# Kernel tuning notes

Measured on AMD Instinct MI355X. Metric: run time of the kernel, lower is better.

## Reference

```python
import jax, jax.numpy as jnp
import numpy as np

N_NODES = 40000            # num nodes (maybe_num_nodes)
E = 2_560_000              # input edges
SENTINEL = N_NODES * N_NODES  # key for masked-out edges; sorts last; fits int32 (1.6e9 < 2^31)


def setup_inputs() -> dict:
    key = jax.random.key(0)
    k1, k2 = jax.random.split(key)
    edge_index = jax.random.randint(k1, (2, E), 0, N_NODES, dtype=jnp.int32)
    edge_attr = jax.random.uniform(k2, (E,), dtype=jnp.float32)
    t = jnp.full((1,), 0.5, dtype=jnp.float32)  # learnable threshold parameter
    return {"edge_index": edge_index, "edge_attr": edge_attr, "t": t}


def reference(edge_index, edge_attr, t):
    """Threshold mask -> symmetrize -> coalesce (sort by (row,col), sum duplicates).

    JAX has static shapes, so compaction is expressed as masking: dropped edges get
    key=SENTINEL (sorts last) and attr contribution 0. Returns padded outputs of
    fixed size 2E plus the count of valid (unique, kept) edges. Invalid slots have
    edge_index == -1 and edge_attr == 0.
    """
    row, col = edge_index[0], edge_index[1]
    mask = edge_attr <= t[0]                      # [E] bool
    # symmetrize: stack (row,col) and (col,row), duplicate attrs  -> [2E]
    r2 = jnp.concatenate([row, col])
    c2 = jnp.concatenate([col, row])
    a2 = jnp.concatenate([edge_attr, edge_attr])
    m2 = jnp.concatenate([mask, mask])
    # coalesce: linearize key = row*N + col, sort, segment-sum duplicates
    key = jnp.where(m2, r2 * N_NODES + c2, SENTINEL)   # [2E] int32
    order = jnp.argsort(key)
    key_s = key[order]
    a_s = jnp.where(m2, a2, 0.0)[order]
    E2 = key_s.shape[0]
    new_seg = jnp.concatenate([jnp.ones((1,), bool), key_s[1:] != key_s[:-1]])
    seg = jnp.cumsum(new_seg.astype(jnp.int32)) - 1    # segment id per sorted edge
    vals = jax.ops.segment_sum(a_s, seg, num_segments=E2, indices_are_sorted=True)
    uk = jnp.full((E2,), SENTINEL, dtype=key_s.dtype).at[seg].set(key_s)
    valid = uk < SENTINEL
    out_row = jnp.where(valid, uk // N_NODES, -1)
    out_col = jnp.where(valid, uk % N_NODES, -1)
    edge_index_out = jnp.stack([out_row, out_col])     # [2, 2E] padded with -1
    edge_attr_out = jnp.where(valid, vals, 0.0)        # [2E]   padded with 0
    num_edges = jnp.sum(valid.astype(jnp.int32))
    return edge_index_out, edge_attr_out, num_edges
```

## Files before the change

kernel.cpp:

```cpp
#include <hip/hip_runtime.h>
#include <stdint.h>

#define NN 40000
#define E_IN 2560000
#define E2 5120000
#define NFINE 2500
#define NSB 20
#define SB_SHIFT 11
#define FINES_PER_SB 128
#define P2_TILES 17
#define P2_TILE 8192
#define SBCAP 135168
#define CAPB 1280
#define CSTR 16
#define P1_BLOCKS 625
#define P1_THREADS 1024
#define OF_BLOCKS 1250

typedef unsigned long long ull;

__global__ void k_init(int* __restrict__ sbCursor, int* __restrict__ fineCursor) {
    int tid = threadIdx.x;
    for (int f = tid; f < NFINE; f += 256) fineCursor[f * CSTR] = f * CAPB;
    if (tid < NSB) sbCursor[tid * CSTR] = tid * SBCAP;
}

__global__ void __launch_bounds__(P1_THREADS) k_part1(const int* __restrict__ ei,
                                                      const float* __restrict__ ea,
                                                      const float* __restrict__ t,
                                                      int* __restrict__ sbCursor,
                                                      ull* __restrict__ pairs1) {
    __shared__ ull staged[8192];
    __shared__ int cntO[NSB * 8];
    __shared__ int off[NSB + 1], wb[NSB * 8], gbase[NSB];
    int tid = threadIdx.x;
    int oct = (tid >> 3) & 7;
    if (tid < NSB * 8) cntO[tid] = 0;
    __syncthreads();
    float t0 = t[0];
    int i0 = blockIdx.x * 4096 + tid * 4;

    float4 a4 = *(const float4*)(ea + i0);
    int4 r4 = *(const int4*)(ei + i0);
    int4 c4 = *(const int4*)(ei + E_IN + i0);
    float av[4] = {a4.x, a4.y, a4.z, a4.w};
    int rv[4] = {r4.x, r4.y, r4.z, r4.w};
    int cv[4] = {c4.x, c4.y, c4.z, c4.w};

    ull eA[4], eB[4];
    int rkA[4], rkB[4];
    bool keep[4];
#pragma unroll
    for (int k = 0; k < 4; k++) {
        keep[k] = (av[k] <= t0);
        if (keep[k]) {
            unsigned ab = __float_as_uint(av[k]);
            eA[k] = ((ull)(unsigned)rv[k] << 48) | ((ull)(unsigned)cv[k] << 32) | ab;
            eB[k] = ((ull)(unsigned)cv[k] << 48) | ((ull)(unsigned)rv[k] << 32) | ab;
            rkA[k] = atomicAdd(&cntO[((rv[k] >> SB_SHIFT) << 3) | oct], 1);
            rkB[k] = atomicAdd(&cntO[((cv[k] >> SB_SHIFT) << 3) | oct], 1);
        }
    }
    __syncthreads();
    if (tid < NSB) {
        int s = tid;
        int c[8], tot = 0;
#pragma unroll
        for (int o = 0; o < 8; o++) { c[o] = cntO[s * 8 + o]; tot += c[o]; }
        int incl = tot;
#pragma unroll
        for (int d = 1; d < 32; d <<= 1) {
            int y = __shfl_up(incl, d, 64);
            if (s >= d) incl += y;
        }
        int o0 = incl - tot;
        off[s] = o0;
        if (s == NSB - 1) off[NSB] = incl;
        int acc = o0;
#pragma unroll
        for (int o = 0; o < 8; o++) { wb[s * 8 + o] = acc; acc += c[o]; }
        gbase[s] = atomicAdd(&sbCursor[s * CSTR], tot);
    }
    __syncthreads();
#pragma unroll
    for (int k = 0; k < 4; k++) {
        if (keep[k]) {
            staged[wb[(((int)(eA[k] >> 59)) << 3) | oct] + rkA[k]] = eA[k];
            staged[wb[(((int)(eB[k] >> 59)) << 3) | oct] + rkB[k]] = eB[k];
        }
    }
    __syncthreads();
    int total = off[NSB];
    for (int i = tid; i < total; i += P1_THREADS) {
        ull e = staged[i];
        int sb = (int)(e >> 59);
        pairs1[gbase[sb] + (i - off[sb])] = e;
    }
}

__global__ void __launch_bounds__(1024) k_part2(const int* __restrict__ sbCursor,
                                                int* __restrict__ fineCursor,
                                                const ull* __restrict__ pairs1,
                                                ull* __restrict__ pairs2) {
    int sb = blockIdx.x / P2_TILES;
    int tile = blockIdx.x % P2_TILES;
    int regionBase = sb * SBCAP;
    int len = sbCursor[sb * CSTR] - regionBase;
    if (len > SBCAP) len = SBCAP;
    int start = tile * P2_TILE;
    if (start >= len) return;
    int cntT = len - start; if (cntT > P2_TILE) cntT = P2_TILE;
    const ull* src = pairs1 + regionBase + start;

    int fineFirst = sb * FINES_PER_SB;
    int nF = NFINE - fineFirst; if (nF > FINES_PER_SB) nF = FINES_PER_SB;

    __shared__ ull staged[P2_TILE];
    __shared__ int cnt[FINES_PER_SB], off[FINES_PER_SB + 1], gbase[FINES_PER_SB], wsum2[2];
    int tid = threadIdx.x;
    if (tid < FINES_PER_SB) { cnt[tid] = 0; gbase[tid] = 0; }
    __syncthreads();

    ull e[8];
    int rk[8];
#pragma unroll
    for (int k = 0; k < 8; k++) {
        int i = tid + k * 1024;
        if (i < cntT) {
            e[k] = src[i];
            rk[k] = atomicAdd(&cnt[(int)(e[k] >> 52) & 127], 1);
        }
    }
    __syncthreads();
    int x = 0, incl = 0;
    if (tid < FINES_PER_SB) {
        x = cnt[tid];
        incl = x;
        int lane = tid & 63;
#pragma unroll
        for (int d = 1; d < 64; d <<= 1) {
            int y = __shfl_up(incl, d, 64);
            if (lane >= d) incl += y;
        }
        if (lane == 63) wsum2[tid >> 6] = incl;
    }
    __syncthreads();
    if (tid == 0) { int a = wsum2[0]; wsum2[0] = 0; wsum2[1] = a; }
    __syncthreads();
    if (tid < FINES_PER_SB) {
        off[tid] = wsum2[tid >> 6] + incl - x;
        if (tid == FINES_PER_SB - 1) off[FINES_PER_SB] = wsum2[1] + incl;
        if (tid < nF) gbase[tid] = atomicAdd(&fineCursor[(fineFirst + tid) * CSTR], x);
    }
    __syncthreads();
#pragma unroll
    for (int k = 0; k < 8; k++) {
        int i = tid + k * 1024;
        if (i < cntT) staged[off[(int)(e[k] >> 52) & 127] + rk[k]] = e[k];
    }
    __syncthreads();
    int total = off[FINES_PER_SB];
    for (int i = tid; i < total; i += 1024) {
        ull v = staged[i];
        int lb = (int)(v >> 52) & 127;
        pairs2[gbase[lb] + (i - off[lb])] = v;
    }
}

__device__ __forceinline__ void ce(ull& a, ull& b) {
    ull mn = a < b ? a : b;
    ull mx = a < b ? b : a;
    a = mn; b = mx;
}
__device__ __forceinline__ void sort8(ull* v) {
    ce(v[0],v[1]); ce(v[2],v[3]); ce(v[4],v[5]); ce(v[6],v[7]);
    ce(v[0],v[2]); ce(v[1],v[3]); ce(v[4],v[6]); ce(v[5],v[7]);
    ce(v[1],v[2]); ce(v[5],v[6]);
    ce(v[0],v[4]); ce(v[1],v[5]); ce(v[2],v[6]); ce(v[3],v[7]);
    ce(v[2],v[4]); ce(v[3],v[5]);
    ce(v[1],v[2]); ce(v[3],v[4]); ce(v[5],v[6]);
}
__device__ __forceinline__ void sort16(ull* v) {
    sort8(v); sort8(v + 8);
    ce(v[0],v[8]);  ce(v[1],v[9]);  ce(v[2],v[10]); ce(v[3],v[11]);
    ce(v[4],v[12]); ce(v[5],v[13]); ce(v[6],v[14]); ce(v[7],v[15]);
    ce(v[4],v[8]);  ce(v[5],v[9]);  ce(v[6],v[10]); ce(v[7],v[11]);
    ce(v[2],v[4]);  ce(v[3],v[5]);  ce(v[6],v[8]);  ce(v[7],v[9]);  ce(v[10],v[12]); ce(v[11],v[13]);
    ce(v[1],v[2]);  ce(v[3],v[4]);  ce(v[5],v[6]);  ce(v[7],v[8]);  ce(v[9],v[10]);  ce(v[11],v[12]); ce(v[13],v[14]);
}

__global__ void __launch_bounds__(512) k_sortrows(const int* __restrict__ fineCursor,
                                                  ull* __restrict__ pairs2,
                                                  int* __restrict__ uniqueCount) {
    int b = blockIdx.x;
    int base = b * CAPB;
    int n = fineCursor[b * CSTR] - base;
    if (n > CAPB) n = CAPB;
    __shared__ ull d[CAPB];
    __shared__ int cnt[512], off[512], wsum[8], ucnt[16], ubase[16];
    int tid = threadIdx.x;
    int lane = tid & 63;
    cnt[tid] = 0;
    __syncthreads();

    ull e[3]; int rk[3], sbk[3];
#pragma unroll
    for (int k = 0; k < 3; k++) {
        int i = tid + k * 512;
        if (i < n) {
            e[k] = pairs2[base + i];
            sbk[k] = (int)(e[k] >> 43) & 511;
            rk[k] = atomicAdd(&cnt[sbk[k]], 1);
        }
    }
    __syncthreads();

    int x = cnt[tid];
    int incl = x;
#pragma unroll
    for (int dlt = 1; dlt < 64; dlt <<= 1) {
        int y = __shfl_up(incl, dlt, 64);
        if (lane >= dlt) incl += y;
    }
    if (lane == 63) wsum[tid >> 6] = incl;
    __syncthreads();
    if (tid == 0) {
        int a = 0;
        for (int w = 0; w < 8; w++) { int tt = wsum[w]; wsum[w] = a; a += tt; }
    }
    __syncthreads();
    off[tid] = wsum[tid >> 6] + incl - x;
    __syncthreads();

#pragma unroll
    for (int k = 0; k < 3; k++) {
        int i = tid + k * 512;
        if (i < n) d[off[sbk[k]] + rk[k]] = e[k];
    }
    __syncthreads();

    int cn = cnt[tid]; if (cn > 16) cn = 16;
    int o0 = off[tid];
    ull v[16];
    bool big = __any(cn > 8);
    if (!big) {
#pragma unroll
        for (int k = 0; k < 8; k++) v[k] = (k < cn) ? d[o0 + k] : ~0ull;
        sort8(v);
    } else {
#pragma unroll
        for (int k = 0; k < 16; k++) v[k] = (k < cn) ? d[o0 + k] : ~0ull;
        sort16(v);
    }

    int uc = (cn > 0) ? 1 : 0;
#pragma unroll
    for (int k = 1; k < 16; k++)
        if (k < cn && (unsigned)(v[k] >> 32) != (unsigned)(v[k - 1] >> 32)) uc++;

    int uincl = uc;
#pragma unroll
    for (int dlt = 1; dlt < 64; dlt <<= 1) {
        int y = __shfl_up(uincl, dlt, 64);
        if (lane >= dlt) uincl += y;
    }
    int rowTot0 = __shfl(uincl, 31, 64);
    int rr = tid >> 5;
    int rowOff = uincl - uc - ((lane >= 32) ? rowTot0 : 0);
    if (lane == 31) ucnt[rr] = uincl;
    if (lane == 63) ucnt[rr] = uincl - rowTot0;
    __syncthreads();
    if (tid == 0) {
        int acc = 0;
        for (int s = 0; s < 16; s++) { ubase[s] = acc; acc += ucnt[s]; }
        uniqueCount[b] = acc;
    }
    __syncthreads();

    if (cn > 0) {
        ull* dst = pairs2 + base + ubase[rr] + rowOff;
        unsigned curKey = (unsigned)(v[0] >> 32);
        float curSum = __uint_as_float((unsigned)v[0]);
        int em = 0;
#pragma unroll
        for (int k = 1; k < 16; k++) {
            if (k < cn) {
                unsigned key = (unsigned)(v[k] >> 32);
                float a = __uint_as_float((unsigned)v[k]);
                if (key == curKey) {
                    curSum += a;
                } else {
                    dst[em] = ((ull)curKey << 32) | __float_as_uint(curSum);
                    em++;
                    curKey = key; curSum = a;
                }
            }
        }
        dst[em] = ((ull)curKey << 32) | __float_as_uint(curSum);
    }
}

__global__ void __launch_bounds__(1024) k_scan(const int* __restrict__ in, int n,
                                               int* __restrict__ outExcl,
                                               float* __restrict__ totalDst) {
    __shared__ int wsum[16];
    int tid = threadIdx.x, lane = tid & 63, w = tid >> 6;
    int start = tid * 3;
    int v[3], sum = 0;
#pragma unroll
    for (int k = 0; k < 3; k++) {
        int i = start + k;
        int x = (i < n) ? in[i] : 0;
        v[k] = sum;
        sum += x;
    }
    int incl = sum;
#pragma unroll
    for (int d = 1; d < 64; d <<= 1) {
        int y = __shfl_up(incl, d, 64);
        if (lane >= d) incl += y;
    }
    if (lane == 63) wsum[w] = incl;
    __syncthreads();
    if (tid < 16) {
        int x2 = wsum[tid];
        int incl2 = x2;
#pragma unroll
        for (int d = 1; d < 16; d <<= 1) {
            int y = __shfl_up(incl2, d, 64);
            if (tid >= d) incl2 += y;
        }
        wsum[tid] = incl2 - x2;
    }
    __syncthreads();
    int base = wsum[w] + incl - sum;
#pragma unroll
    for (int k = 0; k < 3; k++) {
        int i = start + k;
        if (i < n) outExcl[i] = base + v[k];
    }
    if (tid == 1023) {
        int tot = base + sum;
        outExcl[n] = tot;
        if (totalDst) totalDst[0] = (float)tot;
    }
}

__global__ void __launch_bounds__(256) k_outfill(const int* __restrict__ outBase,
                                                 const ull* __restrict__ pairs2,
                                                 float* __restrict__ out) {
    __shared__ int sOB[NFINE + 1];
    int tid = threadIdx.x;
    for (int i = tid; i <= NFINE; i += 256) sOB[i] = outBase[i];
    __syncthreads();
    int T = sOB[NFINE];
    for (int tile = blockIdx.x; tile < E2 / 1024; tile += OF_BLOCKS) {
        int j0 = (tile * 256 + tid) * 4;
        float rr[4], cc[4], aa[4];
        int lo = 0;
        if (j0 < T) {
            int hi = NFINE;
            while (hi - lo > 1) {
                int mid = (lo + hi) >> 1;
                if (sOB[mid] <= j0) lo = mid; else hi = mid;
            }
        }
#pragma unroll
        for (int k = 0; k < 4; k++) {
            int j = j0 + k;
            if (j < T) {
                while (lo < NFINE - 1 && sOB[lo + 1] <= j) lo++;
                ull e = pairs2[lo * CAPB + (j - sOB[lo])];
                rr[k] = (float)(int)(e >> 48);
                cc[k] = (float)(int)((e >> 32) & 0xFFFF);
                aa[k] = __uint_as_float((unsigned)(e & 0xFFFFFFFFu));
            } else { rr[k] = -1.0f; cc[k] = -1.0f; aa[k] = 0.0f; }
        }
        *(float4*)(out + j0)          = make_float4(rr[0], rr[1], rr[2], rr[3]);
        *(float4*)(out + E2 + j0)     = make_float4(cc[0], cc[1], cc[2], cc[3]);
        *(float4*)(out + 2 * E2 + j0) = make_float4(aa[0], aa[1], aa[2], aa[3]);
    }
}

extern "C" void kernel_launch(void* const* d_in, const int* in_sizes, int n_in,
                              void* d_out, int out_size, void* d_ws, size_t ws_size,
                              hipStream_t stream) {
    const int*   ei = (const int*)d_in[0];
    const float* ea = (const float*)d_in[1];
    const float* t  = (const float*)d_in[2];
    float* out = (float*)d_out;

    int* sbCursor    = (int*)d_ws;
    int* fineCursor  = sbCursor + NSB * CSTR;
    int* uniqueCount = fineCursor + NFINE * CSTR;
    int* outBase     = uniqueCount + NFINE;
    ull* pairs2 = (ull*)(((uintptr_t)(outBase + NFINE + 1) + 15) & ~(uintptr_t)15);

    ull* pairs1 = (ull*)d_out;

    k_init<<<1, 256, 0, stream>>>(sbCursor, fineCursor);
    k_part1<<<P1_BLOCKS, P1_THREADS, 0, stream>>>(ei, ea, t, sbCursor, pairs1);
    k_part2<<<NSB * P2_TILES, 1024, 0, stream>>>(sbCursor, fineCursor, pairs1, pairs2);
    k_sortrows<<<NFINE, 512, 0, stream>>>(fineCursor, pairs2, uniqueCount);
    k_scan<<<1, 1024, 0, stream>>>(uniqueCount, NFINE, outBase, out + (size_t)3 * E2);
    k_outfill<<<OF_BLOCKS, 256, 0, stream>>>(outBase, pairs2, out);
}
```

Baseline: 157.2 us.

## Replace atomic superbucket cursors with count-scan pass for deterministic offsets

Adds a counting pass and a single-block scan over per-block histograms, so partition 1 reads precomputed global offsets instead of doing atomicAdd on shared superbucket cursors. This makes the output order within each superbucket deterministic and removes contention on the atomics, at the cost of reading the input twice and launching two extra kernels. The output-fill kernel also changes from a grid-stride loop to contiguous tiles per block, so one binary search per block can be reused across its iterations.

Result: slower. 166.7 us (+6.1%).

```diff
diff --git a/kernel.cpp b/kernel.cpp
--- a/kernel.cpp
+++ b/kernel.cpp
@@ -16,19 +16,72 @@
 #define P1_BLOCKS 625
 #define P1_THREADS 1024
 #define OF_BLOCKS 1250
+#define OF_ITERS 4
 
 typedef unsigned long long ull;
 
-__global__ void k_init(int* __restrict__ sbCursor, int* __restrict__ fineCursor) {
+__global__ void __launch_bounds__(1024) k_count(const int* __restrict__ ei,
+                                                const float* __restrict__ ea,
+                                                const float* __restrict__ t,
+                                                int* __restrict__ hist) {
+    __shared__ int cntO[NSB * 8];
     int tid = threadIdx.x;
-    for (int f = tid; f < NFINE; f += 256) fineCursor[f * CSTR] = f * CAPB;
-    if (tid < NSB) sbCursor[tid * CSTR] = tid * SBCAP;
+    int oct = (tid >> 3) & 7;
+    if (tid < NSB * 8) cntO[tid] = 0;
+    __syncthreads();
+    float t0 = t[0];
+    int i0 = blockIdx.x * 4096 + tid * 4;
+
+    float4 a4 = *(const float4*)(ea + i0);
+    int4 r4 = *(const int4*)(ei + i0);
+    int4 c4 = *(const int4*)(ei + E_IN + i0);
+    float av[4] = {a4.x, a4.y, a4.z, a4.w};
+    int rv[4] = {r4.x, r4.y, r4.z, r4.w};
+    int cv[4] = {c4.x, c4.y, c4.z, c4.w};
+#pragma unroll
+    for (int k = 0; k < 4; k++) {
+        if (av[k] <= t0) {
+            atomicAdd(&cntO[((rv[k] >> SB_SHIFT) << 3) | oct], 1);
+            atomicAdd(&cntO[((cv[k] >> SB_SHIFT) << 3) | oct], 1);
+        }
+    }
+    __syncthreads();
+    if (tid < NSB) {
+        int tot = 0;
+#pragma unroll
+        for (int o = 0; o < 8; o++) tot += cntO[tid * 8 + o];
+        hist[blockIdx.x * NSB + tid] = tot;
+    }
+}
+
+__global__ void __launch_bounds__(1024) k_scanhist(const int* __restrict__ hist,
+                                                   int* __restrict__ baseArr,
+                                                   int* __restrict__ sbLen,
+                                                   int* __restrict__ fineCursor) {
+    int tid = threadIdx.x, lane = tid & 63, w = tid >> 6;
+    for (int s = w; s < NSB; s += 16) {
+        int carry = 0;
+        for (int chunk = 0; chunk < (P1_BLOCKS + 63) / 64; chunk++) {
+            int b = chunk * 64 + lane;
+            int x = (b < P1_BLOCKS) ? hist[b * NSB + s] : 0;
+            int incl = x;
+#pragma unroll
+            for (int d = 1; d < 64; d <<= 1) {
+                int y = __shfl_up(incl, d, 64);
+                if (lane >= d) incl += y;
+            }
+            if (b < P1_BLOCKS) baseArr[b * NSB + s] = s * SBCAP + carry + (incl - x);
+            carry += __shfl(incl, 63, 64);
+        }
+        if (lane == 0) sbLen[s] = carry;
+    }
+    for (int f = tid; f < NFINE; f += 1024) fineCursor[f * CSTR] = f * CAPB;
 }
 
 __global__ void __launch_bounds__(P1_THREADS) k_part1(const int* __restrict__ ei,
                                                       const float* __restrict__ ea,
                                                       const float* __restrict__ t,
-                                                      int* __restrict__ sbCursor,
+                                                      const int* __restrict__ baseArr,
                                                       ull* __restrict__ pairs1) {
     __shared__ ull staged[8192];
     __shared__ int cntO[NSB * 8];
@@ -79,7 +132,7 @@
         int acc = o0;
 #pragma unroll
         for (int o = 0; o < 8; o++) { wb[s * 8 + o] = acc; acc += c[o]; }
-        gbase[s] = atomicAdd(&sbCursor[s * CSTR], tot);
+        gbase[s] = baseArr[blockIdx.x * NSB + s];
     }
     __syncthreads();
 #pragma unroll
@@ -98,14 +151,14 @@
     }
 }
 
-__global__ void __launch_bounds__(1024) k_part2(const int* __restrict__ sbCursor,
+__global__ void __launch_bounds__(1024) k_part2(const int* __restrict__ sbLen,
                                                 int* __restrict__ fineCursor,
                                                 const ull* __restrict__ pairs1,
                                                 ull* __restrict__ pairs2) {
     int sb = blockIdx.x / P2_TILES;
     int tile = blockIdx.x % P2_TILES;
     int regionBase = sb * SBCAP;
-    int len = sbCursor[sb * CSTR] - regionBase;
+    int len = sbLen[sb];
     if (len > SBCAP) len = SBCAP;
     int start = tile * P2_TILE;
     if (start >= len) return;
@@ -354,16 +407,19 @@
     for (int i = tid; i <= NFINE; i += 256) sOB[i] = outBase[i];
     __syncthreads();
     int T = sOB[NFINE];
-    for (int tile = blockIdx.x; tile < E2 / 1024; tile += OF_BLOCKS) {
+    int lo = 0;
+    bool searched = false;
+    for (int it = 0; it < OF_ITERS; it++) {
+        int tile = blockIdx.x * OF_ITERS + it;
         int j0 = (tile * 256 + tid) * 4;
         float rr[4], cc[4], aa[4];
-        int lo = 0;
-        if (j0 < T) {
+        if (j0 < T && !searched) {
             int hi = NFINE;
             while (hi - lo > 1) {
                 int mid = (lo + hi) >> 1;
                 if (sOB[mid] <= j0) lo = mid; else hi = mid;
             }
+            searched = true;
         }
 #pragma unroll
         for (int k = 0; k < 4; k++) {
@@ -390,17 +446,20 @@
     const float* t  = (const float*)d_in[2];
     float* out = (float*)d_out;
 
-    int* sbCursor    = (int*)d_ws;
-    int* fineCursor  = sbCursor + NSB * CSTR;
+    int* sbLen       = (int*)d_ws;
+    int* fineCursor  = sbLen + 32;
     int* uniqueCount = fineCursor + NFINE * CSTR;
     int* outBase     = uniqueCount + NFINE;
-    ull* pairs2 = (ull*)(((uintptr_t)(outBase + NFINE + 1) + 15) & ~(uintptr_t)15);
+    int* hist        = outBase + NFINE + 1;
+    int* baseArr     = hist + P1_BLOCKS * NSB;
+    ull* pairs2 = (ull*)(((uintptr_t)(baseArr + P1_BLOCKS * NSB) + 15) & ~(uintptr_t)15);
 
     ull* pairs1 = (ull*)d_out;
 
-    k_init<<<1, 256, 0, stream>>>(sbCursor, fineCursor);
-    k_part1<<<P1_BLOCKS, P1_THREADS, 0, stream>>>(ei, ea, t, sbCursor, pairs1);
-    k_part2<<<NSB * P2_TILES, 1024, 0, stream>>>(sbCursor, fineCursor, pairs1, pairs2);
+    k_count<<<P1_BLOCKS, P1_THREADS, 0, stream>>>(ei, ea, t, hist);
+    k_scanhist<<<1, 1024, 0, stream>>>(hist, baseArr, sbLen, fineCursor);
+    k_part1<<<P1_BLOCKS, P1_THREADS, 0, stream>>>(ei, ea, t, baseArr, pairs1);
+    k_part2<<<NSB * P2_TILES, 1024, 0, stream>>>(sbLen, fineCursor, pairs1, pairs2);
     k_sortrows<<<NFINE, 512, 0, stream>>>(fineCursor, pairs2, uniqueCount);
     k_scan<<<1, 1024, 0, stream>>>(uniqueCount, NFINE, outBase, out + (size_t)3 * E2);
     k_outfill<<<OF_BLOCKS, 256, 0, stream>>>(outBase, pairs2, out);
```
